# Optimization experiments

Measured on AMD Instinct MI355X. Metric: run time of the kernel, lower is better.

Reference implementation:

```python
import jax, jax.numpy as jnp
import numpy as np

B, T, C = 2, 2048, 1024
NH, H = 16, 64
FF = 3 * C  # feedforward_factor = 3
EPS = 1e-6


def setup_inputs() -> dict:
    key = jax.random.key(0)
    ks = jax.random.split(key, 12)
    s = lambda k, shape, fan: jax.random.normal(k, shape, jnp.float32) * (fan ** -0.5)
    return {
        "x":  jax.random.normal(ks[0], (B, T, C), jnp.float32),
        # per-head projections, stored [nh, C, H] (torch Linear weight [H,C] transposed)
        "Wq": s(ks[1], (NH, C, H), C),
        "Wk": s(ks[2], (NH, C, H), C),
        "Wv": s(ks[3], (NH, C, H), C),
        # combine_heads: torch Linear(nh*H -> C): weight [C, nh*H], bias [C]
        "Wo": s(ks[4], (C, NH * H), NH * H),
        "bo": jnp.zeros((C,), jnp.float32),
        # feedforward
        "W1": s(ks[5], (FF, C), C),
        "b1": jnp.zeros((FF,), jnp.float32),
        "W2": s(ks[6], (C, FF), FF),
        "b2": jnp.zeros((C,), jnp.float32),
        # layer norms (affine)
        "g1": jnp.ones((C,), jnp.float32),
        "be1": jnp.zeros((C,), jnp.float32),
        "g2": jnp.ones((C,), jnp.float32),
        "be2": jnp.zeros((C,), jnp.float32),
    }


def _layernorm(x, gamma, beta):
    # torch: mean / unbiased std (ddof=1), eps added to std (not variance)
    mean = jnp.mean(x, axis=-1, keepdims=True)
    std = jnp.std(x, axis=-1, keepdims=True, ddof=1)
    return gamma * (x - mean) / (std + EPS) + beta


def _attention(xn, Wq, Wk, Wv, Wo, bo):
    q = jnp.einsum("btc,hck->bhtk", xn, Wq)
    k = jnp.einsum("bsc,hck->bhsk", xn, Wk)
    v = jnp.einsum("bsc,hck->bhsk", xn, Wv)
    scores = jnp.einsum("bhtk,bhsk->bhts", q, k) / jnp.sqrt(jnp.float32(H))
    causal = jnp.tril(jnp.ones((T, T), dtype=bool))
    scores = jnp.where(causal, scores, -jnp.inf)
    attn = jax.nn.softmax(scores, axis=-1)
    ctx = jnp.einsum("bhts,bhsk->bhtk", attn, v)
    ctx = jnp.transpose(ctx, (0, 2, 1, 3)).reshape(xn.shape[0], T, NH * H)
    return ctx @ Wo.T + bo


def reference(x, Wq, Wk, Wv, Wo, bo, W1, b1, W2, b2, g1, be1, g2, be2):
    x = x + _attention(_layernorm(x, g1, be1), Wq, Wk, Wv, Wo, bo)
    h = _layernorm(x, g2, be2)
    x = x + (jax.nn.relu(h @ W1.T + b1) @ W2.T + b2)
    return x
```

## Files before the change

### kernel.cpp

```cpp
#include <hip/hip_runtime.h>
#include <stdint.h>

#define Tn   2048
#define Cn   1024
#define NHn  16
#define Hn   64
#define FFn  3072
#define Mrows 4096
#define LNEPS 1e-6f

#if __has_builtin(__builtin_amdgcn_exp2f)
#define EXP2(x) __builtin_amdgcn_exp2f(x)
#else
#define EXP2(x) exp2f(x)
#endif

typedef float f32x4 __attribute__((ext_vector_type(4)));
typedef __bf16 bf16x8 __attribute__((ext_vector_type(8)));
typedef unsigned short us8 __attribute__((ext_vector_type(8)));
typedef unsigned short us4 __attribute__((ext_vector_type(4)));
typedef unsigned int u32x4 __attribute__((ext_vector_type(4)));
typedef unsigned int u32x2 __attribute__((ext_vector_type(2)));

__device__ __forceinline__ unsigned short f2bf(float f) {
    return __builtin_bit_cast(unsigned short, (__bf16)f);
}

__device__ __forceinline__ uint32_t pk2bf(float lo, float hi) {
    return (uint32_t)f2bf(lo) | ((uint32_t)f2bf(hi) << 16);
}

__device__ __forceinline__ void gl_lds16(const void* g, void* l) {
    __builtin_amdgcn_global_load_lds(
        (const __attribute__((address_space(1))) void*)g,
        (__attribute__((address_space(3))) void*)l, 16, 0, 0);
}

#define CQ  (3072 * 1024)
#define CWO (1024 * 1024)
#define CW1 (3072 * 1024)
__global__ __launch_bounds__(256) void cast_all_kernel(
    const float* __restrict__ Wq, const float* __restrict__ Wk,
    const float* __restrict__ Wv, const float* __restrict__ Wo,
    const float* __restrict__ W1, const float* __restrict__ W2,
    unsigned short* __restrict__ wqkv, unsigned short* __restrict__ wo,
    unsigned short* __restrict__ w1,   unsigned short* __restrict__ w2)
{
    int idx = blockIdx.x * 256 + threadIdx.x;
    if (idx < CQ) {
        int n = idx >> 10, cc = idx & 1023;
        const float* W = (n < 1024) ? Wq : ((n < 2048) ? Wk : Wv);
        int nn = n & 1023;
        wqkv[idx] = f2bf(W[(size_t)((nn >> 6) * 1024 + cc) * 64 + (nn & 63)]);
    } else if (idx < CQ + CWO) {
        int j = idx - CQ;
        wo[j] = f2bf(Wo[j]);
    } else if (idx < CQ + CWO + CW1) {
        int j = idx - CQ - CWO;
        w1[j] = f2bf(W1[j]);
    } else {
        int j = idx - CQ - CWO - CW1;
        w2[j] = f2bf(W2[j]);
    }
}

__global__ __launch_bounds__(256) void ln_kernel(
    const float* __restrict__ xin, const float* __restrict__ gamma,
    const float* __restrict__ beta, unsigned short* __restrict__ out)
{
    const int row = blockIdx.x;
    const int tid = threadIdx.x;
    const float4 v = ((const float4*)(xin + (size_t)row * Cn))[tid];
    float s  = v.x + v.y + v.z + v.w;
    float ss = v.x*v.x + v.y*v.y + v.z*v.z + v.w*v.w;
    #pragma unroll
    for (int off = 1; off < 64; off <<= 1) {
        s  += __shfl_xor(s, off);
        ss += __shfl_xor(ss, off);
    }
    __shared__ float red[8];
    const int wave = tid >> 6, lane = tid & 63;
    if (lane == 0) { red[wave] = s; red[4 + wave] = ss; }
    __syncthreads();
    float S  = red[0] + red[1] + red[2] + red[3];
    float SS = red[4] + red[5] + red[6] + red[7];
    float mean = S * (1.0f / 1024.0f);
    float var  = (SS - 1024.0f * mean * mean) * (1.0f / 1023.0f);
    var = fmaxf(var, 0.0f);
    float inv = 1.0f / (sqrtf(var) + LNEPS);
    const float4 gv = ((const float4*)gamma)[tid];
    const float4 bv = ((const float4*)beta)[tid];
    us4 ov;
    ov[0] = f2bf(gv.x * (v.x - mean) * inv + bv.x);
    ov[1] = f2bf(gv.y * (v.y - mean) * inv + bv.y);
    ov[2] = f2bf(gv.z * (v.z - mean) * inv + bv.z);
    ov[3] = f2bf(gv.w * (v.w - mean) * inv + bv.w);
    *(us4*)(out + (size_t)row * Cn + tid * 4) = ov;
}

template<int MODE>
__global__ __launch_bounds__(512) void gemm_bt(
    const unsigned short* __restrict__ A,
    const unsigned short* __restrict__ Bt,
    void* Cout,
    const float* __restrict__ bias,
    const float* resid,
    int M, int N, int K)
{
    __shared__ unsigned short lds[3][8192];
    const int tid  = threadIdx.x;
    const int wave = tid >> 6, lane = tid & 63;
    const int g = lane >> 4, c = lane & 15;
    const int wr = wave >> 2, wc = wave & 3;
    const int m0 = blockIdx.x * 128, n0 = blockIdx.y * 128;

    f32x4 acc[4][2];
    #pragma unroll
    for (int i = 0; i < 4; i++)
        #pragma unroll
        for (int j = 0; j < 2; j++) acc[i][j] = (f32x4){0.f, 0.f, 0.f, 0.f};

    const int srow = wave * 16 + (lane >> 2);
    const int scol = (((lane & 3) ^ ((lane >> 3) & 3)) * 8);
    const unsigned short* sA = A  + (size_t)(m0 + srow) * K + scol;
    const unsigned short* sB = Bt + (size_t)(n0 + srow) * K + scol;
    const int wdst = wave * 512;

    auto STAGE = [&](int t, int b) {
        const int ko = t * 32;
        gl_lds16(sA + ko, &lds[b][wdst]);
        gl_lds16(sB + ko, &lds[b][4096 + wdst]);
    };

    STAGE(0, 0);
    STAGE(1, 1);
    asm volatile("s_waitcnt vmcnt(2)" ::: "memory");
    __builtin_amdgcn_s_barrier();

    const int jsw = (g ^ ((c >> 1) & 3)) * 8;

    const int NT = K >> 5;
    int cur = 0;
    for (int t = 0; t < NT; ++t) {
        const bool pf = (t + 2 < NT);
        if (pf) { int b = cur + 2; if (b >= 3) b -= 3; STAGE(t + 2, b); }

        bf16x8 af[4], bfr[2];
        #pragma unroll
        for (int mi = 0; mi < 4; mi++)
            af[mi]  = *(const bf16x8*)&lds[cur][(wr * 64 + mi * 16 + c) * 32 + jsw];
        #pragma unroll
        for (int ni = 0; ni < 2; ni++)
            bfr[ni] = *(const bf16x8*)&lds[cur][4096 + (wc * 32 + ni * 16 + c) * 32 + jsw];
        __builtin_amdgcn_s_setprio(1);
        #pragma unroll
        for (int mi = 0; mi < 4; mi++)
            #pragma unroll
            for (int ni = 0; ni < 2; ni++)
                acc[mi][ni] = __builtin_amdgcn_mfma_f32_16x16x32_bf16(
                    af[mi], bfr[ni], acc[mi][ni], 0, 0, 0);
        __builtin_amdgcn_s_setprio(0);

        if (pf) asm volatile("s_waitcnt vmcnt(2)" ::: "memory");
        else    asm volatile("s_waitcnt vmcnt(0)" ::: "memory");
        __builtin_amdgcn_s_barrier();
        cur = (cur == 2) ? 0 : cur + 1;
    }

    const int rowb = m0 + wr * 64 + g * 4;
    const int colb = n0 + wc * 32 + c;
    #pragma unroll
    for (int mi = 0; mi < 4; mi++) {
        #pragma unroll
        for (int ni = 0; ni < 2; ni++) {
            const int col = colb + ni * 16;
            float bv = (MODE == 1 || MODE == 2) ? bias[col] : 0.f;
            #pragma unroll
            for (int r = 0; r < 4; r++) {
                const int row = rowb + mi * 16 + r;
                float v = acc[mi][ni][r];
                if (MODE == 1) {
                    float res = resid[(size_t)row * N + col];
                    ((float*)Cout)[(size_t)row * N + col] = v + bv + res;
                } else if (MODE == 2) {
                    float t = v + bv;
                    t = t > 0.f ? t : 0.f;
                    ((unsigned short*)Cout)[(size_t)row * N + col] = f2bf(t);
                } else {
                    ((unsigned short*)Cout)[(size_t)row * N + col] = f2bf(v);
                }
            }
        }
    }
}

__global__ __launch_bounds__(256) void transpose_v_kernel(
    const unsigned short* __restrict__ qkv, unsigned short* __restrict__ vt)
{
    __shared__ unsigned short tile[64][72];
    const int bh = blockIdx.y;
    const int b = bh >> 4, h = bh & 15;
    const int t0 = blockIdx.x * 64;
    const int tid = threadIdx.x;
    const int tr = tid >> 2;
    const int dc = (tid & 3) * 16;
    const unsigned short* src =
        qkv + (size_t)(b * Tn + t0 + tr) * 3072 + 2048 + h * 64 + dc;
    *(us8*)&tile[tr][dc]     = *(const us8*)src;
    *(us8*)&tile[tr][dc + 8] = *(const us8*)(src + 8);
    __syncthreads();
    const int dr = tid >> 2;
    const int tc = (tid & 3) * 16;
    unsigned short* dst = vt + (size_t)bh * Hn * Tn + (size_t)dr * Tn + t0 + tc;
    us8 o0, o1;
    #pragma unroll
    for (int e = 0; e < 8; e++) o0[e] = tile[tc + e][dr];
    #pragma unroll
    for (int e = 0; e < 8; e++) o1[e] = tile[tc + 8 + e][dr];
    *(us8*)dst       = o0;
    *(us8*)(dst + 8) = o1;
}

__global__ __launch_bounds__(128, 2) void attn_kernel(
    const unsigned short* __restrict__ qkv,
    const unsigned short* __restrict__ vt,
    unsigned short* __restrict__ ctx)
{
    const float SCL = 0.125f * 1.44269504088896f;
    __shared__ float Osh[2][4][64][4];
    __shared__ float Msh[2][64];
    __shared__ float Lsh[2][64];
    __shared__ uint32_t Psh[2][2][16][36];

    const int tid  = threadIdx.x;
    const int wave = tid >> 6, lane = tid & 63;
    const int g = lane >> 4, c = lane & 15;
    const int l = blockIdx.x;
    const int pj = l >> 5;
    const int bh = ((l & 7) << 2) | ((l >> 3) & 3);
    const int b = bh >> 4, h = bh & 15;
    const unsigned short* base  = qkv + (size_t)b * Tn * 3072;
    const unsigned short* qbase = base + h * 64;
    const unsigned short* kbase = base + 1024 + h * 64;
    const unsigned short* vtb   = vt + (size_t)bh * (Hn * Tn);

    for (int half = 0; half < 2; ++half) {
        const int tileIdx = half ? (63 - pj) : pj;
        const int t0 = tileIdx * 32;
        const int nch  = (t0 + 95) >> 6;
        const int nh0  = (nch + 1) >> 1;
        const int cbeg = wave ? nh0 : 0;
        const int cend = wave ? nch : nh0;

        bf16x8 qf[2][2];
        #pragma unroll
        for (int qa = 0; qa < 2; qa++) {
            const unsigned short* qp = qbase + (size_t)(t0 + qa * 16 + c) * 3072 + g * 8;
            qf[qa][0] = *(const bf16x8*)qp;
            qf[qa][1] = *(const bf16x8*)(qp + 32);
        }

        float mrun[2] = {-1e30f, -1e30f};
        float lrun[2] = {0.f, 0.f};
        f32x4 o[2][4];
        #pragma unroll
        for (int qa = 0; qa < 2; qa++)
            #pragma unroll
            for (int nc = 0; nc < 4; nc++) o[qa][nc] = (f32x4){0.f, 0.f, 0.f, 0.f};

        for (int ci = cbeg; ci < cend; ++ci) {
            const int s0 = ci * 64;
            bf16x8 kf[4][2];
            #pragma unroll
            for (int sc = 0; sc < 4; sc++) {
                const unsigned short* kp = kbase + (size_t)(s0 + sc * 16 + c) * 3072 + g * 8;
                kf[sc][0] = *(const bf16x8*)kp;
                kf[sc][1] = *(const bf16x8*)(kp + 32);
            }
            bf16x8 vf[4][2];
            #pragma unroll
            for (int nc = 0; nc < 4; nc++)
                #pragma unroll
                for (int ks = 0; ks < 2; ks++)
                    vf[nc][ks] = *(const bf16x8*)(vtb + (size_t)(nc * 16 + c) * Tn
                                                  + s0 + ks * 32 + g * 8);

            f32x4 sacc[2][4];
            #pragma unroll
            for (int qa = 0; qa < 2; qa++)
                #pragma unroll
                for (int sc = 0; sc < 4; sc++) {
                    f32x4 z = (f32x4){0.f, 0.f, 0.f, 0.f};
                    z = __builtin_amdgcn_mfma_f32_16x16x32_bf16(kf[sc][0], qf[qa][0], z, 0, 0, 0);
                    z = __builtin_amdgcn_mfma_f32_16x16x32_bf16(kf[sc][1], qf[qa][1], z, 0, 0, 0);
                    sacc[qa][sc] = z;
                }

            uint32_t dw[2][4][2];
            #pragma unroll
            for (int qa = 0; qa < 2; qa++) {
                const int q = t0 + qa * 16 + c;
                float pm[4][4];
                const bool needMask = (s0 + 63 > t0 + qa * 16);
                #pragma unroll
                for (int sc = 0; sc < 4; sc++)
                    #pragma unroll
                    for (int r = 0; r < 4; r++) {
                        float v = sacc[qa][sc][r] * SCL;
                        if (needMask && (s0 + sc * 16 + 4 * g + r > q)) v = -1e30f;
                        pm[sc][r] = v;
                    }
                float tmax = pm[0][0];
                #pragma unroll
                for (int sc = 0; sc < 4; sc++)
                    #pragma unroll
                    for (int r = 0; r < 4; r++) tmax = fmaxf(tmax, pm[sc][r]);
                tmax = fmaxf(tmax, __shfl_xor(tmax, 16));
                tmax = fmaxf(tmax, __shfl_xor(tmax, 32));
                if (!__all(tmax - mrun[qa] <= 8.0f)) {
                    float mnew = fmaxf(mrun[qa], tmax);
                    float corr = EXP2(mrun[qa] - mnew);
                    mrun[qa] = mnew;
                    lrun[qa] *= corr;
                    float cb[4];
                    #pragma unroll
                    for (int r = 0; r < 4; r++) cb[r] = __shfl(corr, 4 * g + r);
                    #pragma unroll
                    for (int nc = 0; nc < 4; nc++)
                        #pragma unroll
                        for (int r = 0; r < 4; r++) o[qa][nc][r] *= cb[r];
                }
                float csum = 0.f;
                #pragma unroll
                for (int sc = 0; sc < 4; sc++)
                    #pragma unroll
                    for (int r = 0; r < 4; r++) {
                        float p = EXP2(pm[sc][r] - mrun[qa]);
                        pm[sc][r] = p;
                        csum += p;
                    }
                csum += __shfl_xor(csum, 16);
                csum += __shfl_xor(csum, 32);
                lrun[qa] += csum;
                #pragma unroll
                for (int sc = 0; sc < 4; sc++) {
                    dw[qa][sc][0] = pk2bf(pm[sc][0], pm[sc][1]);
                    dw[qa][sc][1] = pk2bf(pm[sc][2], pm[sc][3]);
                }
            }

            #pragma unroll
            for (int qa = 0; qa < 2; qa++)
                #pragma unroll
                for (int sc = 0; sc < 4; sc++) {
                    u32x2 wv = { dw[qa][sc][0], dw[qa][sc][1] };
                    *(u32x2*)&Psh[wave][qa][c][sc * 8 + 2 * g] = wv;
                }
            #pragma unroll
            for (int ks = 0; ks < 2; ks++) {
                #pragma unroll
                for (int qa = 0; qa < 2; qa++) {
                    u32x4 pd = *(const u32x4*)&Psh[wave][qa][c][ks * 16 + 4 * g];
                    bf16x8 pa = __builtin_bit_cast(bf16x8, pd);
                    #pragma unroll
                    for (int nc = 0; nc < 4; nc++)
                        o[qa][nc] = __builtin_amdgcn_mfma_f32_16x16x32_bf16(
                            pa, vf[nc][ks], o[qa][nc], 0, 0, 0);
                }
            }
        }

        f32x4 oS[4], oX[4];
        float mS, lS, mX, lX;
        if (wave == 0) {
            #pragma unroll
            for (int nc = 0; nc < 4; nc++) { oS[nc] = o[0][nc]; oX[nc] = o[1][nc]; }
            mS = mrun[0]; lS = lrun[0]; mX = mrun[1]; lX = lrun[1];
        } else {
            #pragma unroll
            for (int nc = 0; nc < 4; nc++) { oS[nc] = o[1][nc]; oX[nc] = o[0][nc]; }
            mS = mrun[1]; lS = lrun[1]; mX = mrun[0]; lX = lrun[0];
        }
        #pragma unroll
        for (int nc = 0; nc < 4; nc++)
            *(f32x4*)&Osh[wave][nc][lane][0] = oX[nc];
        Msh[wave][lane] = mX;
        Lsh[wave][lane] = lX;
        __syncthreads();
        const int pw = wave ^ 1;
        float mP = Msh[pw][lane];
        float lP = Lsh[pw][lane];
        float mM = fmaxf(mS, mP);
        float cS = EXP2(mS - mM);
        float cP = EXP2(mP - mM);
        float rl = 1.0f / (lS * cS + lP * cP);
        float cbS[4], cbP[4], lb[4];
        #pragma unroll
        for (int r = 0; r < 4; r++) {
            cbS[r] = __shfl(cS, 4 * g + r);
            cbP[r] = __shfl(cP, 4 * g + r);
            lb[r]  = __shfl(rl, 4 * g + r);
        }
        #pragma unroll
        for (int nc = 0; nc < 4; nc++) {
            f32x4 oP = *(const f32x4*)&Osh[pw][nc][lane][0];
            #pragma unroll
            for (int r = 0; r < 4; r++) {
                const int trow = t0 + wave * 16 + 4 * g + r;
                float val = (oS[nc][r] * cbS[r] + oP[r] * cbP[r]) * lb[r];
                ctx[(size_t)(b * Tn + trow) * 1024 + h * 64 + nc * 16 + c] = f2bf(val);
            }
        }
        __syncthreads();
    }
}

extern "C" void kernel_launch(void* const* d_in, const int* in_sizes, int n_in,
                              void* d_out, int out_size, void* d_ws, size_t ws_size,
                              hipStream_t stream) {
    const float* x   = (const float*)d_in[0];
    const float* Wq  = (const float*)d_in[1];
    const float* Wk  = (const float*)d_in[2];
    const float* Wv  = (const float*)d_in[3];
    const float* Wo  = (const float*)d_in[4];
    const float* bo  = (const float*)d_in[5];
    const float* W1  = (const float*)d_in[6];
    const float* b1  = (const float*)d_in[7];
    const float* W2  = (const float*)d_in[8];
    const float* b2  = (const float*)d_in[9];
    const float* g1  = (const float*)d_in[10];
    const float* be1 = (const float*)d_in[11];
    const float* g2  = (const float*)d_in[12];
    const float* be2 = (const float*)d_in[13];

    char* ws = (char*)d_ws;
    unsigned short* wqkv = (unsigned short*)ws;  ws += (size_t)3072 * 1024 * 2;
    unsigned short* wo   = (unsigned short*)ws;  ws += (size_t)1024 * 1024 * 2;
    unsigned short* w1   = (unsigned short*)ws;  ws += (size_t)3072 * 1024 * 2;
    unsigned short* w2   = (unsigned short*)ws;  ws += (size_t)1024 * 3072 * 2;
    unsigned short* bufA = (unsigned short*)ws;  ws += (size_t)Mrows * 1024 * 2;
    unsigned short* bufB = (unsigned short*)ws;  ws += (size_t)Mrows * 3072 * 2;

    float* xout = (float*)d_out;
    unsigned short* vt = (unsigned short*)d_out;

    cast_all_kernel<<<40960, 256, 0, stream>>>(Wq, Wk, Wv, Wo, W1, W2,
                                               wqkv, wo, w1, w2);

    ln_kernel<<<Mrows, 256, 0, stream>>>(x, g1, be1, bufA);
    gemm_bt<0><<<dim3(32, 24), 512, 0, stream>>>(bufA, wqkv, bufB, nullptr, nullptr,
                                                 Mrows, 3072, 1024);
    transpose_v_kernel<<<dim3(Tn / 64, 2 * NHn), 256, 0, stream>>>(bufB, vt);
    attn_kernel<<<dim3(1024), 128, 0, stream>>>(bufB, vt, bufA);
    gemm_bt<1><<<dim3(32, 8), 512, 0, stream>>>(bufA, wo, xout, bo, x,
                                                Mrows, 1024, 1024);
    ln_kernel<<<Mrows, 256, 0, stream>>>(xout, g2, be2, bufA);
    gemm_bt<2><<<dim3(32, 24), 512, 0, stream>>>(bufA, w1, bufB, b1, nullptr,
                                                 Mrows, 3072, 1024);
    gemm_bt<1><<<dim3(32, 8), 512, 0, stream>>>(bufB, w2, xout, b2, (const float*)xout,
                                                Mrows, 1024, 3072);
}
```

Baseline: 235.8 us.

## Add 64x128-tile residual GEMM for N=1024 projections; make softmax rescale unconditional

```diff
diff --git a/kernel.cpp b/kernel.cpp
--- a/kernel.cpp
+++ b/kernel.cpp
@@ -194,6 +194,94 @@
     }
 }
 
+__global__ __launch_bounds__(256) void gemm_bt64(
+    const unsigned short* __restrict__ A,
+    const unsigned short* __restrict__ Bt,
+    void* Cout,
+    const float* __restrict__ bias,
+    const float* resid,
+    int M, int N, int K)
+{
+    __shared__ unsigned short lds[3][6144];
+    const int tid  = threadIdx.x;
+    const int wave = tid >> 6, lane = tid & 63;
+    const int g = lane >> 4, c = lane & 15;
+    const int wc = wave;
+    const int m0 = blockIdx.x * 64, n0 = blockIdx.y * 128;
+
+    f32x4 acc[4][2];
+    #pragma unroll
+    for (int i = 0; i < 4; i++)
+        #pragma unroll
+        for (int j = 0; j < 2; j++) acc[i][j] = (f32x4){0.f, 0.f, 0.f, 0.f};
+
+    const int srow = tid >> 2;
+    const int scol = (((tid & 3) ^ ((tid >> 3) & 3)) * 8);
+    const unsigned short* sA  = A  + (size_t)(m0 + srow)      * K + scol;
+    const unsigned short* sB0 = Bt + (size_t)(n0 + srow)      * K + scol;
+    const unsigned short* sB1 = Bt + (size_t)(n0 + 64 + srow) * K + scol;
+    const int d8 = tid * 8;
+
+    auto STAGE = [&](int t, int b) {
+        const int ko = t * 32;
+        gl_lds16(sA  + ko, &lds[b][d8]);
+        gl_lds16(sB0 + ko, &lds[b][2048 + d8]);
+        gl_lds16(sB1 + ko, &lds[b][4096 + d8]);
+    };
+
+    STAGE(0, 0);
+    STAGE(1, 1);
+    asm volatile("s_waitcnt vmcnt(3)" ::: "memory");
+    __builtin_amdgcn_s_barrier();
+
+    const int jsw = (g ^ ((c >> 1) & 3)) * 8;
+
+    const int NT = K >> 5;
+    int cur = 0;
+    for (int t = 0; t < NT; ++t) {
+        const bool pf = (t + 2 < NT);
+        if (pf) { int b = cur + 2; if (b >= 3) b -= 3; STAGE(t + 2, b); }
+
+        bf16x8 af[4], bfr[2];
+        #pragma unroll
+        for (int mi = 0; mi < 4; mi++)
+            af[mi]  = *(const bf16x8*)&lds[cur][(mi * 16 + c) * 32 + jsw];
+        #pragma unroll
+        for (int ni = 0; ni < 2; ni++)
+            bfr[ni] = *(const bf16x8*)&lds[cur][2048 + (wc * 32 + ni * 16 + c) * 32 + jsw];
+        __builtin_amdgcn_s_setprio(1);
+        #pragma unroll
+        for (int mi = 0; mi < 4; mi++)
+            #pragma unroll
+            for (int ni = 0; ni < 2; ni++)
+                acc[mi][ni] = __builtin_amdgcn_mfma_f32_16x16x32_bf16(
+                    af[mi], bfr[ni], acc[mi][ni], 0, 0, 0);
+        __builtin_amdgcn_s_setprio(0);
+
+        if (pf) asm volatile("s_waitcnt vmcnt(3)" ::: "memory");
+        else    asm volatile("s_waitcnt vmcnt(0)" ::: "memory");
+        __builtin_amdgcn_s_barrier();
+        cur = (cur == 2) ? 0 : cur + 1;
+    }
+
+    const int rowb = m0 + g * 4;
+    const int colb = n0 + wc * 32 + c;
+    #pragma unroll
+    for (int mi = 0; mi < 4; mi++) {
+        #pragma unroll
+        for (int ni = 0; ni < 2; ni++) {
+            const int col = colb + ni * 16;
+            float bv = bias[col];
+            #pragma unroll
+            for (int r = 0; r < 4; r++) {
+                const int row = rowb + mi * 16 + r;
+                float res = resid[(size_t)row * N + col];
+                ((float*)Cout)[(size_t)row * N + col] = acc[mi][ni][r] + bv + res;
+            }
+        }
+    }
+}
+
 __global__ __launch_bounds__(256) void transpose_v_kernel(
     const unsigned short* __restrict__ qkv, unsigned short* __restrict__ vt)
 {
@@ -317,31 +405,28 @@
                     for (int r = 0; r < 4; r++) tmax = fmaxf(tmax, pm[sc][r]);
                 tmax = fmaxf(tmax, __shfl_xor(tmax, 16));
                 tmax = fmaxf(tmax, __shfl_xor(tmax, 32));
-                if (!__all(tmax - mrun[qa] <= 8.0f)) {
-                    float mnew = fmaxf(mrun[qa], tmax);
-                    float corr = EXP2(mrun[qa] - mnew);
-                    mrun[qa] = mnew;
-                    lrun[qa] *= corr;
-                    float cb[4];
-                    #pragma unroll
-                    for (int r = 0; r < 4; r++) cb[r] = __shfl(corr, 4 * g + r);
-                    #pragma unroll
-                    for (int nc = 0; nc < 4; nc++)
-                        #pragma unroll
-                        for (int r = 0; r < 4; r++) o[qa][nc][r] *= cb[r];
-                }
+                float mnew = fmaxf(mrun[qa], tmax);
+                float corr = EXP2(mrun[qa] - mnew);
+                mrun[qa] = mnew;
                 float csum = 0.f;
                 #pragma unroll
                 for (int sc = 0; sc < 4; sc++)
                     #pragma unroll
                     for (int r = 0; r < 4; r++) {
-                        float p = EXP2(pm[sc][r] - mrun[qa]);
+                        float p = EXP2(pm[sc][r] - mnew);
                         pm[sc][r] = p;
                         csum += p;
                     }
                 csum += __shfl_xor(csum, 16);
                 csum += __shfl_xor(csum, 32);
-                lrun[qa] += csum;
+                lrun[qa] = lrun[qa] * corr + csum;
+                float cb[4];
+                #pragma unroll
+                for (int r = 0; r < 4; r++) cb[r] = __shfl(corr, 4 * g + r);
+                #pragma unroll
+                for (int nc = 0; nc < 4; nc++)
+                    #pragma unroll
+                    for (int r = 0; r < 4; r++) o[qa][nc][r] *= cb[r];
                 #pragma unroll
                 for (int sc = 0; sc < 4; sc++) {
                     dw[qa][sc][0] = pk2bf(pm[sc][0], pm[sc][1]);
@@ -452,11 +537,11 @@
                                                  Mrows, 3072, 1024);
     transpose_v_kernel<<<dim3(Tn / 64, 2 * NHn), 256, 0, stream>>>(bufB, vt);
     attn_kernel<<<dim3(1024), 128, 0, stream>>>(bufB, vt, bufA);
-    gemm_bt<1><<<dim3(32, 8), 512, 0, stream>>>(bufA, wo, xout, bo, x,
-                                                Mrows, 1024, 1024);
+    gemm_bt64<<<dim3(64, 8), 256, 0, stream>>>(bufA, wo, xout, bo, x,
+                                               Mrows, 1024, 1024);
     ln_kernel<<<Mrows, 256, 0, stream>>>(xout, g2, be2, bufA);
     gemm_bt<2><<<dim3(32, 24), 512, 0, stream>>>(bufA, w1, bufB, b1, nullptr,
                                                  Mrows, 3072, 1024);
-    gemm_bt<1><<<dim3(32, 8), 512, 0, stream>>>(bufB, w2, xout, b2, (const float*)xout,
-                                                Mrows, 1024, 3072);
-}
+    gemm_bt64<<<dim3(64, 8), 256, 0, stream>>>(bufB, w2, xout, b2, (const float*)xout,
+                                               Mrows, 1024, 3072);
+}
```

Measured after the change: 245.6 us. +4.1%, slower.
